# Kernel optimization log

Measured on AMD Instinct MI355X. Metric: run time of the kernel, lower is better.

## Reference

```python
import jax, jax.numpy as jnp
import numpy as np

B, T, H = 32, 500, 1612            # 6 regions * 256 + iti 76
ALM_EXC_LO, ALM_EXC_HI = 1280, 1460  # alm starts at 5*256; exc = 0.7*256 = 180 units
T_CONST = 0.1


def _base_firing():
    # per-region base firing rates: str 0, gpe 0.8, stn 0.5, snr 0.8, thal 0.8, alm 0, iti 0
    sizes = [256, 256, 256, 256, 256, 256, 76]
    rates = [0.0, 0.8, 0.5, 0.8, 0.8, 0.0, 0.0]
    return jnp.asarray(np.concatenate([np.full(s, r, np.float32) for s, r in zip(sizes, rates)]))


def setup_inputs() -> dict:
    key = jax.random.key(0)
    ks = jax.random.split(key, 12)
    inp = jax.random.normal(ks[0], (B, T, 1), jnp.float32)
    cue_inp = jax.random.normal(ks[1], (B, T, 1), jnp.float32)
    hn = jax.random.uniform(ks[2], (1, B, H), jnp.float32)
    xn = 0.1 * jax.random.normal(ks[3], (1, B, H), jnp.float32)
    inhib_stim = 0.01 * jax.random.normal(ks[4], (B, T, H), jnp.float32)
    W_rec = jax.random.uniform(ks[5], (H, H), jnp.float32, 0.0, 0.01)
    # binary connectivity mask (stands in for the sparse/cell-type block masks)
    W_rec_mask = (jax.random.uniform(ks[6], (H, H), jnp.float32) < 0.5).astype(jnp.float32)
    W_rec_fixed = jnp.zeros((H, H), jnp.float32)
    # diagonal +/-1 sign matrix (Dale's law), kept as a full matrix as in the source
    signs = jnp.where(jax.random.uniform(ks[7], (H,), jnp.float32) < 0.5, -1.0, 1.0)
    W_rec_sign = jnp.diag(signs)
    W_inp = jax.random.uniform(ks[8], (H, 1), jnp.float32, 0.0, 0.01)
    W_cue = jax.random.uniform(ks[9], (H, 1), jnp.float32, 0.0, 0.01)
    out_weight_alm = (1.0 / 256.0) * jnp.ones((1, ALM_EXC_HI - ALM_EXC_LO), jnp.float32)
    base_firing = _base_firing()
    return {"inp": inp, "cue_inp": cue_inp, "hn": hn, "xn": xn, "inhib_stim": inhib_stim,
            "W_rec": W_rec, "W_rec_mask": W_rec_mask, "W_rec_fixed": W_rec_fixed,
            "W_rec_sign": W_rec_sign, "W_inp": W_inp, "W_cue": W_cue,
            "out_weight_alm": out_weight_alm, "base_firing": base_firing}


def reference(inp, cue_inp, hn, xn, inhib_stim, W_rec, W_rec_mask, W_rec_fixed,
              W_rec_sign, W_inp, W_cue, out_weight_alm, base_firing):
    # Dale's-law constrained effective recurrent weights:
    # (mask * hardtanh(W, 0, 1) + fixed) @ sign
    W_eff = (W_rec_mask * jnp.clip(W_rec, 0.0, 1.0) + W_rec_fixed) @ W_rec_sign  # [H,H]
    x0 = xn[0]  # [B,H]
    h0 = hn[0]  # [B,H]

    def step(carry, ts):
        x, h = carry
        i_t, c_t, s_t = ts  # [B,1],[B,1],[B,H]
        ff = h @ W_eff.T + i_t @ W_inp.T + c_t @ W_cue.T + s_t
        x_new = x + T_CONST * (-x + ff)
        h_new = jax.nn.relu(x_new + base_firing)
        return (x_new, h_new), h_new

    ts = (jnp.transpose(inp, (1, 0, 2)), jnp.transpose(cue_inp, (1, 0, 2)),
          jnp.transpose(inhib_stim, (1, 0, 2)))
    _, hs = jax.lax.scan(step, (x0, h0), ts)  # hs: [T,B,H]
    out = hs[:, :, ALM_EXC_LO:ALM_EXC_HI] @ out_weight_alm.T  # [T,B,out_dim]
    return jnp.transpose(out, (1, 0, 2))  # [B,T,out_dim]
```

## Files before the change

### kernel.cpp

```cpp
#include <hip/hip_runtime.h>

#define BB 32
#define TT 500
#define HH 1612
#define HP 1664
#define HR 1624
#define NW 16
#define THREADS 1024
#define NWG 256
#define RPW 8
#define KPW (HP / NW)
#define ALO 1280
#define AHI 1460
#define WSTR 1668
#define RSTR 36
#define HBUF (HP * BB)
#define T_CONST 0.1f


__global__ void pers_init(const float* __restrict__ hn, const float* __restrict__ Wsign,
                          float* __restrict__ out, float* __restrict__ hbase,
                          float* __restrict__ sdiag, unsigned* __restrict__ cnt)
{
    const int gid = blockIdx.x * blockDim.x + threadIdx.x;
    const int gsz = gridDim.x * blockDim.x;
    for (int i = gid; i < HP; i += gsz)
        sdiag[i] = (i < HH) ? Wsign[(size_t)i * HH + i] : 0.f;
    for (int i = gid; i < HP * BB; i += gsz) {
        const int k = i >> 5, b = i & 31;
        hbase[(k >> 2) * 128 + b * 4 + (k & 3)] = (k < HH) ? hn[b * HH + k] : 0.f;
    }
    for (int i = gid; i < TT * 13 * 128; i += gsz) {
        const int buf = 1 + i / (13 * 128);
        const int off = i % (13 * 128);
        hbase[(size_t)buf * HBUF + 403 * 128 + off] = 0.f;
    }
    for (int i = gid; i < BB * TT; i += gsz) out[i] = 0.f;
    for (int i = gid; i < 512; i += gsz) cnt[i] = 0u;
}

__global__ __launch_bounds__(THREADS, 1) void pers_kernel(
    const float* __restrict__ xn,
    const float* __restrict__ Wrec, const float* __restrict__ Wmask,
    const float* __restrict__ Wfix, const float* __restrict__ sdiag,
    const float* __restrict__ inp,  const float* __restrict__ cue,
    const float* __restrict__ stim, const float* __restrict__ Winp,
    const float* __restrict__ Wcue, const float* __restrict__ walm,
    const float* __restrict__ base, float* __restrict__ out,
    float* __restrict__ hbase,      unsigned* __restrict__ cnt)
{
    __shared__ float Wlds[RPW * WSTR];
    __shared__ float red[NW * RPW * RSTR];
    __shared__ float almb[RPW * RSTR];

    const int tid  = threadIdx.x;
    const int wg   = blockIdx.x;
    const int wave = tid >> 6;
    const int lane = tid & 63;
    const int bl   = lane & 15;
    const int rq   = (lane >> 4) & 3;

    const int r0    = (wg * HH) / NWG;
    const int r1    = ((wg + 1) * HH) / NWG;
    const int nreal = r1 - r0;

    for (int i = tid; i < RPW * (HP / 4); i += THREADS) {
        const int r = i / (HP / 4), k = (i % (HP / 4)) * 4;
        const int j = r0 + r;
        float4 v = make_float4(0.f, 0.f, 0.f, 0.f);
        if (r < nreal && k < HH) {
            const float4 w = *(const float4*)&Wrec[(size_t)j * HH + k];
            const float4 m = *(const float4*)&Wmask[(size_t)j * HH + k];
            const float4 f = *(const float4*)&Wfix[(size_t)j * HH + k];
            const float4 s = *(const float4*)&sdiag[k];
            v.x = (m.x * fminf(fmaxf(w.x, 0.f), 1.f) + f.x) * s.x;
            v.y = (m.y * fminf(fmaxf(w.y, 0.f), 1.f) + f.y) * s.y;
            v.z = (m.z * fminf(fmaxf(w.z, 0.f), 1.f) + f.z) * s.z;
            v.w = (m.w * fminf(fmaxf(w.w, 0.f), 1.f) + f.w) * s.w;
        }
        *(float4*)&Wlds[r * WSTR + k] = v;
    }

    const int er = tid & 7, eb = tid >> 3;
    const int ej = r0 + er;
    const bool eactive = (tid < 256) && (er < nreal);
    float xv = 0.f, basej = 0.f, winpj = 0.f, wcuej = 0.f, walmj = 0.f;
    if (eactive) {
        xv    = xn[eb * HH + ej];
        basej = base[ej];
        winpj = Winp[ej];
        wcuej = Wcue[ej];
        walmj = (ej >= ALO && ej < AHI) ? walm[ej - ALO] : 0.f;
    }
    const bool has_alm = (r1 > ALO) && (r0 < AHI);
    const int kbase = wave * KPW;

    __syncthreads();

    for (int t = 0; t < TT; ++t) {
        const float* __restrict__ hc = hbase + (size_t)t * HBUF;
        float* __restrict__ hx       = hbase + (size_t)(t + 1) * HBUF;

        float sv = 0.f, iv = 0.f, cv = 0.f;
        if (eactive) {
            sv = __builtin_nontemporal_load(
                     &stim[(size_t)eb * (TT * HH) + (size_t)t * HH + ej]);
            iv = inp[eb * TT + t];
            cv = cue[eb * TT + t];
        }

        float a00 = 0.f, a01 = 0.f, a10 = 0.f, a11 = 0.f;
        {
            const float* __restrict__ hq  = hc + kbase * BB + bl * 4;
            const float* __restrict__ w0p = &Wlds[rq * WSTR + kbase];
            const float* __restrict__ w1p = w0p + 4 * WSTR;
            #pragma unroll 2
            for (int q = 0; q < KPW / 4; ++q) {
                const float4 h0 = *(const float4*)(hq + q * 128);
                const float4 h1 = *(const float4*)(hq + q * 128 + 64);
                const float4 w0 = *(const float4*)(w0p + q * 4);
                const float4 w1 = *(const float4*)(w1p + q * 4);
                a00 = fmaf(w0.x, h0.x, a00); a00 = fmaf(w0.y, h0.y, a00);
                a00 = fmaf(w0.z, h0.z, a00); a00 = fmaf(w0.w, h0.w, a00);
                a01 = fmaf(w0.x, h1.x, a01); a01 = fmaf(w0.y, h1.y, a01);
                a01 = fmaf(w0.z, h1.z, a01); a01 = fmaf(w0.w, h1.w, a01);
                a10 = fmaf(w1.x, h0.x, a10); a10 = fmaf(w1.y, h0.y, a10);
                a10 = fmaf(w1.z, h0.z, a10); a10 = fmaf(w1.w, h0.w, a10);
                a11 = fmaf(w1.x, h1.x, a11); a11 = fmaf(w1.y, h1.y, a11);
                a11 = fmaf(w1.z, h1.z, a11); a11 = fmaf(w1.w, h1.w, a11);
            }
        }

        red[(wave * RPW + rq    ) * RSTR + bl     ] = a00;
        red[(wave * RPW + rq    ) * RSTR + bl + 16] = a01;
        red[(wave * RPW + rq + 4) * RSTR + bl     ] = a10;
        red[(wave * RPW + rq + 4) * RSTR + bl + 16] = a11;
        __syncthreads();

        float av = 0.f;
        if (tid < 256) {
            float ff = 0.f;
            #pragma unroll
            for (int w2 = 0; w2 < NW; ++w2)
                ff += red[(w2 * RPW + er) * RSTR + eb];
            if (eactive) {
                ff += sv;
                ff = fmaf(iv, winpj, ff);
                ff = fmaf(cv, wcuej, ff);
                xv = fmaf(T_CONST, ff - xv, xv);
                const float hval = fmaxf(xv + basej, 0.f);
                __hip_atomic_store(&hx[(ej >> 2) * 128 + eb * 4 + (ej & 3)], hval,
                                   __ATOMIC_RELAXED, __HIP_MEMORY_SCOPE_AGENT);
                av = hval * walmj;
            }
        }

        if (has_alm) {
            if (tid < 256) almb[er * RSTR + eb] = av;
            __syncthreads();
            if (tid < 32) {
                float s8 = 0.f;
                #pragma unroll
                for (int r = 0; r < RPW; ++r) s8 += almb[r * RSTR + tid];
                atomicAdd(&out[tid * TT + t], s8);
            }
        }

        if (t != TT - 1) {
            __syncthreads();
            if (tid == 0)
                __hip_atomic_fetch_add(&cnt[(wg & 7) << 6], 1u,
                                       __ATOMIC_RELAXED, __HIP_MEMORY_SCOPE_AGENT);
            if (wave == 0) {
                const unsigned target = 256u * (unsigned)(t + 1);
                unsigned s;
                do {
                    __builtin_amdgcn_s_sleep(1);
                    unsigned v = (lane < 8)
                        ? __hip_atomic_load(&cnt[lane << 6], __ATOMIC_RELAXED,
                                            __HIP_MEMORY_SCOPE_AGENT)
                        : 0u;
                    v += __shfl_xor(v, 1);
                    v += __shfl_xor(v, 2);
                    v += __shfl_xor(v, 4);
                    s = __shfl(v, 0);
                } while (s < target);
            }
            __syncthreads();
        }
    }
}


#define FTHREADS 512
#define FNW 8
#define FKPW (HP / FNW)

__global__ void init_kernel(const float* __restrict__ hn, const float* __restrict__ xn,
                            const float* __restrict__ Wsign, float* __restrict__ out,
                            float* __restrict__ hA, float* __restrict__ xs,
                            float* __restrict__ sdiag)
{
    const int gid = blockIdx.x * blockDim.x + threadIdx.x;
    const int gsz = gridDim.x * blockDim.x;
    for (int i = gid; i < HP; i += gsz)
        sdiag[i] = (i < HH) ? Wsign[(size_t)i * HH + i] : 0.f;
    for (int i = gid; i < HP * BB; i += gsz) {
        const int k = i >> 5, b = i & 31;
        hA[(k >> 2) * (BB * 4) + b * 4 + (k & 3)] = (k < HH) ? hn[b * HH + k] : 0.f;
    }
    for (int i = gid; i < HH * BB; i += gsz) {
        const int j = i >> 5, b = i & 31;
        xs[i] = xn[b * HH + j];
    }
    for (int i = gid; i < BB * TT; i += gsz) out[i] = 0.f;
}

__global__ void weff_kernel(const float* __restrict__ Wrec, const float* __restrict__ Wmask,
                            const float* __restrict__ Wfix, const float* __restrict__ sdiag,
                            float* __restrict__ Weff)
{
    const int gid = blockIdx.x * blockDim.x + threadIdx.x;
    const int gsz = gridDim.x * blockDim.x;
    const int nq = HR * (HP / 4);
    for (int qi = gid; qi < nq; qi += gsz) {
        const int j = qi / (HP / 4);
        const int k = (qi % (HP / 4)) * 4;
        float4 v = make_float4(0.f, 0.f, 0.f, 0.f);
        if (j < HH && k < HH) {
            const float4 w = *(const float4*)&Wrec[(size_t)j * HH + k];
            const float4 m = *(const float4*)&Wmask[(size_t)j * HH + k];
            const float4 f = *(const float4*)&Wfix[(size_t)j * HH + k];
            const float4 s = *(const float4*)&sdiag[k];
            v.x = (m.x * fminf(fmaxf(w.x, 0.f), 1.f) + f.x) * s.x;
            v.y = (m.y * fminf(fmaxf(w.y, 0.f), 1.f) + f.y) * s.y;
            v.z = (m.z * fminf(fmaxf(w.z, 0.f), 1.f) + f.z) * s.z;
            v.w = (m.w * fminf(fmaxf(w.w, 0.f), 1.f) + f.w) * s.w;
        }
        *(float4*)&Weff[(size_t)j * HP + k] = v;
    }
}

template <bool PRE>
__global__ __launch_bounds__(FTHREADS, 1) void step_kernel(
    const int t,
    const float* __restrict__ hc,  float* __restrict__ hnx,
    float* __restrict__ xs,        const float* __restrict__ Weff,
    const float* __restrict__ Wrec,const float* __restrict__ Wmask,
    const float* __restrict__ Wfix,const float* __restrict__ sdiag,
    const float* __restrict__ inp, const float* __restrict__ cue,
    const float* __restrict__ stim,const float* __restrict__ Winp,
    const float* __restrict__ Wcue,const float* __restrict__ walm,
    const float* __restrict__ base,float* __restrict__ out)
{
    __shared__ float Wlds[RPW * WSTR];
    __shared__ float red[FNW * RPW * RSTR];
    __shared__ float almb[RPW * RSTR];

    const int tid  = threadIdx.x;
    const int wg   = blockIdx.x;
    const int wave = tid >> 6;
    const int lane = tid & 63;
    const int bl   = lane & 15;
    const int rq   = (lane >> 4) & 3;

    const int r0    = (wg * HH) / NWG;
    const int r1    = ((wg + 1) * HH) / NWG;
    const int nreal = r1 - r0;

    const int er = tid & 7, eb = tid >> 3;
    const int ej = r0 + er;
    const bool eactive = (tid < 256) && (er < nreal);
    float sv = 0.f, iv = 0.f, cv = 0.f, xv = 0.f;
    float basej = 0.f, winpj = 0.f, wcuej = 0.f, walmj = 0.f;
    if (eactive) {
        sv    = __builtin_nontemporal_load(
                    &stim[(size_t)eb * (TT * HH) + (size_t)t * HH + ej]);
        iv    = inp[eb * TT + t];
        cv    = cue[eb * TT + t];
        xv    = xs[ej * BB + eb];
        basej = base[ej];
        winpj = Winp[ej];
        wcuej = Wcue[ej];
        walmj = (ej >= ALO && ej < AHI) ? walm[ej - ALO] : 0.f;
    }
    const bool has_alm = (r1 > ALO) && (r0 < AHI);

    if constexpr (PRE) {
        for (int i = tid; i < RPW * (HP / 4); i += FTHREADS) {
            const int r = i / (HP / 4), k = (i % (HP / 4)) * 4;
            const float4 v = *(const float4*)&Weff[(size_t)(r0 + r) * HP + k];
            *(float4*)&Wlds[r * WSTR + k] = v;
        }
    } else {
        for (int i = tid; i < RPW * (HP / 4); i += FTHREADS) {
            const int r = i / (HP / 4), k = (i % (HP / 4)) * 4;
            const int j = r0 + r;
            float4 v = make_float4(0.f, 0.f, 0.f, 0.f);
            if (r < nreal && k < HH) {
                const float4 w = *(const float4*)&Wrec[(size_t)j * HH + k];
                const float4 m = *(const float4*)&Wmask[(size_t)j * HH + k];
                const float4 f = *(const float4*)&Wfix[(size_t)j * HH + k];
                const float4 s = *(const float4*)&sdiag[k];
                v.x = (m.x * fminf(fmaxf(w.x, 0.f), 1.f) + f.x) * s.x;
                v.y = (m.y * fminf(fmaxf(w.y, 0.f), 1.f) + f.y) * s.y;
                v.z = (m.z * fminf(fmaxf(w.z, 0.f), 1.f) + f.z) * s.z;
                v.w = (m.w * fminf(fmaxf(w.w, 0.f), 1.f) + f.w) * s.w;
            }
            *(float4*)&Wlds[r * WSTR + k] = v;
        }
    }
    __syncthreads();

    float a00 = 0.f, a01 = 0.f, a10 = 0.f, a11 = 0.f;
    {
        const int kbase = wave * FKPW;
        const float* __restrict__ hq  = hc + kbase * BB + bl * 4;
        const float* __restrict__ w0p = &Wlds[rq * WSTR + kbase];
        const float* __restrict__ w1p = w0p + 4 * WSTR;
        #pragma unroll 4
        for (int q = 0; q < FKPW / 4; ++q) {
            const float4 h0 = *(const float4*)(hq + q * 128);
            const float4 h1 = *(const float4*)(hq + q * 128 + 64);
            const float4 w0 = *(const float4*)(w0p + q * 4);
            const float4 w1 = *(const float4*)(w1p + q * 4);
            a00 = fmaf(w0.x, h0.x, a00); a00 = fmaf(w0.y, h0.y, a00);
            a00 = fmaf(w0.z, h0.z, a00); a00 = fmaf(w0.w, h0.w, a00);
            a01 = fmaf(w0.x, h1.x, a01); a01 = fmaf(w0.y, h1.y, a01);
            a01 = fmaf(w0.z, h1.z, a01); a01 = fmaf(w0.w, h1.w, a01);
            a10 = fmaf(w1.x, h0.x, a10); a10 = fmaf(w1.y, h0.y, a10);
            a10 = fmaf(w1.z, h0.z, a10); a10 = fmaf(w1.w, h0.w, a10);
            a11 = fmaf(w1.x, h1.x, a11); a11 = fmaf(w1.y, h1.y, a11);
            a11 = fmaf(w1.z, h1.z, a11); a11 = fmaf(w1.w, h1.w, a11);
        }
    }

    red[(wave * RPW + rq    ) * RSTR + bl     ] = a00;
    red[(wave * RPW + rq    ) * RSTR + bl + 16] = a01;
    red[(wave * RPW + rq + 4) * RSTR + bl     ] = a10;
    red[(wave * RPW + rq + 4) * RSTR + bl + 16] = a11;
    __syncthreads();

    float av = 0.f;
    if (tid < 256) {
        float ff = 0.f;
        #pragma unroll
        for (int w2 = 0; w2 < FNW; ++w2)
            ff += red[(w2 * RPW + er) * RSTR + eb];
        if (eactive) {
            ff += sv;
            ff = fmaf(iv, winpj, ff);
            ff = fmaf(cv, wcuej, ff);
            xv = fmaf(T_CONST, ff - xv, xv);
            xs[ej * BB + eb] = xv;
            const float hval = fmaxf(xv + basej, 0.f);
            hnx[(ej >> 2) * (BB * 4) + eb * 4 + (ej & 3)] = hval;
            av = hval * walmj;
        }
    }

    if (has_alm) {
        if (tid < 256) almb[er * RSTR + eb] = av;
        __syncthreads();
        if (tid < 32) {
            float s8 = 0.f;
            #pragma unroll
            for (int r = 0; r < RPW; ++r) s8 += almb[r * RSTR + tid];
            atomicAdd(&out[tid * TT + t], s8);
        }
    }
}

extern "C" void kernel_launch(void* const* d_in, const int* in_sizes, int n_in,
                              void* d_out, int out_size, void* d_ws, size_t ws_size,
                              hipStream_t stream) {
    const float* inp   = (const float*)d_in[0];
    const float* cue   = (const float*)d_in[1];
    const float* hn    = (const float*)d_in[2];
    const float* xn    = (const float*)d_in[3];
    const float* stim  = (const float*)d_in[4];
    const float* Wrec  = (const float*)d_in[5];
    const float* Wmask = (const float*)d_in[6];
    const float* Wfix  = (const float*)d_in[7];
    const float* Wsign = (const float*)d_in[8];
    const float* Winp  = (const float*)d_in[9];
    const float* Wcue  = (const float*)d_in[10];
    const float* walm  = (const float*)d_in[11];
    const float* base  = (const float*)d_in[12];
    float* out = (float*)d_out;

    const size_t pers_need = ((size_t)(TT + 1) * HBUF + HP) * sizeof(float) + 2048;
    if (ws_size >= pers_need) {
        float* hbase    = (float*)d_ws;
        float* sdiag    = hbase + (size_t)(TT + 1) * HBUF;
        unsigned* cnt   = (unsigned*)(sdiag + HP);

        pers_init<<<NWG, 256, 0, stream>>>(hn, Wsign, out, hbase, sdiag, cnt);

        void* args[] = { (void*)&xn, (void*)&Wrec, (void*)&Wmask, (void*)&Wfix,
                         (void*)&sdiag, (void*)&inp, (void*)&cue, (void*)&stim,
                         (void*)&Winp, (void*)&Wcue, (void*)&walm, (void*)&base,
                         (void*)&out, (void*)&hbase, (void*)&cnt };
        hipLaunchCooperativeKernel(reinterpret_cast<void*>(pers_kernel),
                                   dim3(NWG), dim3(THREADS), args, 0, stream);
        return;
    }

    const size_t weff_elems = (size_t)HR * HP;
    const size_t need = (weff_elems + 3 * (size_t)HP * BB + HP) * sizeof(float);
    const bool pre = (ws_size >= need);

    float* Weff, *hA, *hB, *xs, *sdiag;
    if (pre) {
        Weff  = (float*)d_ws;
        hA    = Weff + weff_elems;
    } else {
        Weff  = nullptr;
        hA    = (float*)d_ws;
    }
    hB    = hA + (size_t)HP * BB;
    xs    = hB + (size_t)HP * BB;
    sdiag = xs + (size_t)HP * BB;

    init_kernel<<<NWG, 256, 0, stream>>>(hn, xn, Wsign, out, hA, xs, sdiag);
    if (pre)
        weff_kernel<<<NWG, 256, 0, stream>>>(Wrec, Wmask, Wfix, sdiag, Weff);

    float* hc = hA;
    float* hx = hB;
    for (int t = 0; t < TT; ++t) {
        if (pre)
            step_kernel<true><<<NWG, FTHREADS, 0, stream>>>(
                t, hc, hx, xs, Weff, nullptr, nullptr, nullptr, nullptr,
                inp, cue, stim, Winp, Wcue, walm, base, out);
        else
            step_kernel<false><<<NWG, FTHREADS, 0, stream>>>(
                t, hc, hx, xs, nullptr, Wrec, Wmask, Wfix, sdiag,
                inp, cue, stim, Winp, Wcue, walm, base, out);
        float* tmp = hc; hc = hx; hx = tmp;
    }
}
```

Baseline: 5.199 ms.

## Keep recurrent weights in registers and reduce partial sums with wave shuffles

Each thread now holds a 4-row by 13-column slice of the effective recurrent weights in registers, instead of the workgroup staging 8 rows in LDS. The hidden-state buffer moves to a plain k-major [k][b] layout, and each thread reads 8 batch values per k. Partial sums are first combined with cross-lane shuffles, then with an LDS reduction over k-slices. The grid-barrier arrive is issued earlier and the sleep in the spin-wait is removed, to cut LDS traffic and barrier latency. Padding rows of later h buffers are no longer zeroed, so any non-finite garbage left in the workspace could leak into the sums. Register pressure also rises.

After: 14.14 ms. 172% more time.

```diff
diff --git a/kernel.cpp b/kernel.cpp
--- a/kernel.cpp
+++ b/kernel.cpp
@@ -5,17 +5,22 @@
 #define HH 1612
 #define HP 1664
 #define HR 1624
-#define NW 16
+#define NWG 256
 #define THREADS 1024
-#define NWG 256
-#define RPW 8
-#define KPW (HP / NW)
 #define ALO 1280
 #define AHI 1460
+#define T_CONST 0.1f
+#define HBUFS (HP * BB)
+#define KSL 208
+#define KL 13
+#define RED_STR 36
+
 #define WSTR 1668
 #define RSTR 36
-#define HBUF (HP * BB)
-#define T_CONST 0.1f
+#define RPW 8
+#define FTHREADS 512
+#define FNW 8
+#define FKPW (HP / FNW)
 
 
 __global__ void pers_init(const float* __restrict__ hn, const float* __restrict__ Wsign,
@@ -26,15 +31,12 @@
     const int gsz = gridDim.x * blockDim.x;
     for (int i = gid; i < HP; i += gsz)
         sdiag[i] = (i < HH) ? Wsign[(size_t)i * HH + i] : 0.f;
-    for (int i = gid; i < HP * BB; i += gsz) {
+    for (int i = gid; i < HH * BB; i += gsz) {
         const int k = i >> 5, b = i & 31;
-        hbase[(k >> 2) * 128 + b * 4 + (k & 3)] = (k < HH) ? hn[b * HH + k] : 0.f;
-    }
-    for (int i = gid; i < TT * 13 * 128; i += gsz) {
-        const int buf = 1 + i / (13 * 128);
-        const int off = i % (13 * 128);
-        hbase[(size_t)buf * HBUF + 403 * 128 + off] = 0.f;
-    }
+        hbase[k * BB + b] = hn[b * HH + k];
+    }
+    for (int i = gid; i < (HP - HH) * BB; i += gsz)
+        hbase[HH * BB + i] = 0.f;
     for (int i = gid; i < BB * TT; i += gsz) out[i] = 0.f;
     for (int i = gid; i < 512; i += gsz) cnt[i] = 0u;
 }
@@ -49,39 +51,41 @@
     const float* __restrict__ base, float* __restrict__ out,
     float* __restrict__ hbase,      unsigned* __restrict__ cnt)
 {
-    __shared__ float Wlds[RPW * WSTR];
-    __shared__ float red[NW * RPW * RSTR];
-    __shared__ float almb[RPW * RSTR];
+    __shared__ float red[256 * RED_STR];
+    __shared__ float almb[8 * 33];
 
     const int tid  = threadIdx.x;
     const int wg   = blockIdx.x;
     const int wave = tid >> 6;
     const int lane = tid & 63;
-    const int bl   = lane & 15;
-    const int rq   = (lane >> 4) & 3;
+    const int rh   = wave >> 3;
+    const int ks   = wave & 7;
+    const int kg   = lane >> 2;
+    const int bg   = lane & 3;
 
     const int r0    = (wg * HH) / NWG;
     const int r1    = ((wg + 1) * HH) / NWG;
     const int nreal = r1 - r0;
 
-    for (int i = tid; i < RPW * (HP / 4); i += THREADS) {
-        const int r = i / (HP / 4), k = (i % (HP / 4)) * 4;
-        const int j = r0 + r;
-        float4 v = make_float4(0.f, 0.f, 0.f, 0.f);
-        if (r < nreal && k < HH) {
-            const float4 w = *(const float4*)&Wrec[(size_t)j * HH + k];
-            const float4 m = *(const float4*)&Wmask[(size_t)j * HH + k];
-            const float4 f = *(const float4*)&Wfix[(size_t)j * HH + k];
-            const float4 s = *(const float4*)&sdiag[k];
-            v.x = (m.x * fminf(fmaxf(w.x, 0.f), 1.f) + f.x) * s.x;
-            v.y = (m.y * fminf(fmaxf(w.y, 0.f), 1.f) + f.y) * s.y;
-            v.z = (m.z * fminf(fmaxf(w.z, 0.f), 1.f) + f.z) * s.z;
-            v.w = (m.w * fminf(fmaxf(w.w, 0.f), 1.f) + f.w) * s.w;
-        }
-        *(float4*)&Wlds[r * WSTR + k] = v;
-    }
-
-    const int er = tid & 7, eb = tid >> 3;
+    const int k0 = ks * KSL + kg * KL;
+    float W[4][KL];
+    #pragma unroll
+    for (int rr = 0; rr < 4; ++rr) {
+        const int j = r0 + rh * 4 + rr;
+        #pragma unroll
+        for (int i = 0; i < KL; ++i) {
+            const int k = k0 + i;
+            float v = 0.f;
+            if (j < HH && k < HH) {
+                float w = Wrec[(size_t)j * HH + k];
+                w = fminf(fmaxf(w, 0.f), 1.f);
+                v = (Wmask[(size_t)j * HH + k] * w + Wfix[(size_t)j * HH + k]) * sdiag[k];
+            }
+            W[rr][i] = v;
+        }
+    }
+
+    const int er = tid >> 5, eb = tid & 31;
     const int ej = r0 + er;
     const bool eactive = (tid < 256) && (er < nreal);
     float xv = 0.f, basej = 0.f, winpj = 0.f, wcuej = 0.f, walmj = 0.f;
@@ -93,13 +97,14 @@
         walmj = (ej >= ALO && ej < AHI) ? walm[ej - ALO] : 0.f;
     }
     const bool has_alm = (r1 > ALO) && (r0 < AHI);
-    const int kbase = wave * KPW;
+    const int erh = er >> 2, err = er & 3;
+    const int off0 = k0 * BB + bg * 8;
 
     __syncthreads();
 
     for (int t = 0; t < TT; ++t) {
-        const float* __restrict__ hc = hbase + (size_t)t * HBUF;
-        float* __restrict__ hx       = hbase + (size_t)(t + 1) * HBUF;
+        const float* __restrict__ hc = hbase + (size_t)t * HBUFS;
+        float* __restrict__ hx       = hbase + (size_t)(t + 1) * HBUFS;
 
         float sv = 0.f, iv = 0.f, cv = 0.f;
         if (eactive) {
@@ -109,73 +114,95 @@
             cv = cue[eb * TT + t];
         }
 
-        float a00 = 0.f, a01 = 0.f, a10 = 0.f, a11 = 0.f;
-        {
-            const float* __restrict__ hq  = hc + kbase * BB + bl * 4;
-            const float* __restrict__ w0p = &Wlds[rq * WSTR + kbase];
-            const float* __restrict__ w1p = w0p + 4 * WSTR;
-            #pragma unroll 2
-            for (int q = 0; q < KPW / 4; ++q) {
-                const float4 h0 = *(const float4*)(hq + q * 128);
-                const float4 h1 = *(const float4*)(hq + q * 128 + 64);
-                const float4 w0 = *(const float4*)(w0p + q * 4);
-                const float4 w1 = *(const float4*)(w1p + q * 4);
-                a00 = fmaf(w0.x, h0.x, a00); a00 = fmaf(w0.y, h0.y, a00);
-                a00 = fmaf(w0.z, h0.z, a00); a00 = fmaf(w0.w, h0.w, a00);
-                a01 = fmaf(w0.x, h1.x, a01); a01 = fmaf(w0.y, h1.y, a01);
-                a01 = fmaf(w0.z, h1.z, a01); a01 = fmaf(w0.w, h1.w, a01);
-                a10 = fmaf(w1.x, h0.x, a10); a10 = fmaf(w1.y, h0.y, a10);
-                a10 = fmaf(w1.z, h0.z, a10); a10 = fmaf(w1.w, h0.w, a10);
-                a11 = fmaf(w1.x, h1.x, a11); a11 = fmaf(w1.y, h1.y, a11);
-                a11 = fmaf(w1.z, h1.z, a11); a11 = fmaf(w1.w, h1.w, a11);
-            }
-        }
-
-        red[(wave * RPW + rq    ) * RSTR + bl     ] = a00;
-        red[(wave * RPW + rq    ) * RSTR + bl + 16] = a01;
-        red[(wave * RPW + rq + 4) * RSTR + bl     ] = a10;
-        red[(wave * RPW + rq + 4) * RSTR + bl + 16] = a11;
+        float acc[4][8];
+        #pragma unroll
+        for (int rr = 0; rr < 4; ++rr)
+            #pragma unroll
+            for (int bb = 0; bb < 8; ++bb) acc[rr][bb] = 0.f;
+
+        const float* __restrict__ hp = hc + off0;
+        #pragma unroll
+        for (int i = 0; i < KL; ++i) {
+            const float4 ha = *(const float4*)(hp + i * BB);
+            const float4 hb = *(const float4*)(hp + i * BB + 4);
+            #pragma unroll
+            for (int rr = 0; rr < 4; ++rr) {
+                const float w = W[rr][i];
+                acc[rr][0] = fmaf(w, ha.x, acc[rr][0]);
+                acc[rr][1] = fmaf(w, ha.y, acc[rr][1]);
+                acc[rr][2] = fmaf(w, ha.z, acc[rr][2]);
+                acc[rr][3] = fmaf(w, ha.w, acc[rr][3]);
+                acc[rr][4] = fmaf(w, hb.x, acc[rr][4]);
+                acc[rr][5] = fmaf(w, hb.y, acc[rr][5]);
+                acc[rr][6] = fmaf(w, hb.z, acc[rr][6]);
+                acc[rr][7] = fmaf(w, hb.w, acc[rr][7]);
+            }
+        }
+
+        #pragma unroll
+        for (int rr = 0; rr < 4; ++rr)
+            #pragma unroll
+            for (int bb = 0; bb < 8; ++bb) {
+                float v = acc[rr][bb];
+                v += __shfl_xor(v, 4);
+                v += __shfl_xor(v, 8);
+                acc[rr][bb] = v;
+            }
+
+        if ((lane & 12) == 0) {
+            const int kq = lane >> 4;
+            #pragma unroll
+            for (int rr = 0; rr < 4; ++rr) {
+                const int row = wave * 16 + kq * 4 + rr;
+                *(float4*)&red[row * RED_STR + bg * 8] =
+                    make_float4(acc[rr][0], acc[rr][1], acc[rr][2], acc[rr][3]);
+                *(float4*)&red[row * RED_STR + bg * 8 + 4] =
+                    make_float4(acc[rr][4], acc[rr][5], acc[rr][6], acc[rr][7]);
+            }
+        }
         __syncthreads();
 
         float av = 0.f;
         if (tid < 256) {
             float ff = 0.f;
             #pragma unroll
-            for (int w2 = 0; w2 < NW; ++w2)
-                ff += red[(w2 * RPW + er) * RSTR + eb];
+            for (int ksx = 0; ksx < 8; ++ksx)
+                #pragma unroll
+                for (int kq = 0; kq < 4; ++kq)
+                    ff += red[((erh * 8 + ksx) * 16 + kq * 4 + err) * RED_STR + eb];
             if (eactive) {
                 ff += sv;
                 ff = fmaf(iv, winpj, ff);
                 ff = fmaf(cv, wcuej, ff);
                 xv = fmaf(T_CONST, ff - xv, xv);
                 const float hval = fmaxf(xv + basej, 0.f);
-                __hip_atomic_store(&hx[(ej >> 2) * 128 + eb * 4 + (ej & 3)], hval,
+                __hip_atomic_store(&hx[ej * BB + eb], hval,
                                    __ATOMIC_RELAXED, __HIP_MEMORY_SCOPE_AGENT);
                 av = hval * walmj;
             }
-        }
+            if (has_alm) almb[er * 33 + eb] = av;
+        }
+
+        __syncthreads();
+
+        if (tid == 0)
+            __hip_atomic_fetch_add(&cnt[(wg & 7) << 6], 1u,
+                                   __ATOMIC_RELAXED, __HIP_MEMORY_SCOPE_AGENT);
 
         if (has_alm) {
-            if (tid < 256) almb[er * RSTR + eb] = av;
-            __syncthreads();
             if (tid < 32) {
                 float s8 = 0.f;
                 #pragma unroll
-                for (int r = 0; r < RPW; ++r) s8 += almb[r * RSTR + tid];
+                for (int r = 0; r < 8; ++r) s8 += almb[r * 33 + tid];
                 atomicAdd(&out[tid * TT + t], s8);
             }
         }
 
         if (t != TT - 1) {
-            __syncthreads();
-            if (tid == 0)
-                __hip_atomic_fetch_add(&cnt[(wg & 7) << 6], 1u,
-                                       __ATOMIC_RELAXED, __HIP_MEMORY_SCOPE_AGENT);
             if (wave == 0) {
                 const unsigned target = 256u * (unsigned)(t + 1);
                 unsigned s;
                 do {
-                    __builtin_amdgcn_s_sleep(1);
                     unsigned v = (lane < 8)
                         ? __hip_atomic_load(&cnt[lane << 6], __ATOMIC_RELAXED,
                                             __HIP_MEMORY_SCOPE_AGENT)
@@ -191,10 +218,6 @@
     }
 }
 
-
-#define FTHREADS 512
-#define FNW 8
-#define FKPW (HP / FNW)
 
 __global__ void init_kernel(const float* __restrict__ hn, const float* __restrict__ xn,
                             const float* __restrict__ Wsign, float* __restrict__ out,
@@ -254,8 +277,8 @@
     const float* __restrict__ base,float* __restrict__ out)
 {
     __shared__ float Wlds[RPW * WSTR];
-    __shared__ float red[FNW * RPW * RSTR];
-    __shared__ float almb[RPW * RSTR];
+    __shared__ float red2[FNW * RPW * RSTR];
+    __shared__ float almb2[RPW * RSTR];
 
     const int tid  = threadIdx.x;
     const int wg   = blockIdx.x;
@@ -335,10 +358,10 @@
         }
     }
 
-    red[(wave * RPW + rq    ) * RSTR + bl     ] = a00;
-    red[(wave * RPW + rq    ) * RSTR + bl + 16] = a01;
-    red[(wave * RPW + rq + 4) * RSTR + bl     ] = a10;
-    red[(wave * RPW + rq + 4) * RSTR + bl + 16] = a11;
+    red2[(wave * RPW + rq    ) * RSTR + bl     ] = a00;
+    red2[(wave * RPW + rq    ) * RSTR + bl + 16] = a01;
+    red2[(wave * RPW + rq + 4) * RSTR + bl     ] = a10;
+    red2[(wave * RPW + rq + 4) * RSTR + bl + 16] = a11;
     __syncthreads();
 
     float av = 0.f;
@@ -346,7 +369,7 @@
         float ff = 0.f;
         #pragma unroll
         for (int w2 = 0; w2 < FNW; ++w2)
-            ff += red[(w2 * RPW + er) * RSTR + eb];
+            ff += red2[(w2 * RPW + er) * RSTR + eb];
         if (eactive) {
             ff += sv;
             ff = fmaf(iv, winpj, ff);
@@ -360,12 +383,12 @@
     }
 
     if (has_alm) {
-        if (tid < 256) almb[er * RSTR + eb] = av;
+        if (tid < 256) almb2[er * RSTR + eb] = av;
         __syncthreads();
         if (tid < 32) {
             float s8 = 0.f;
             #pragma unroll
-            for (int r = 0; r < RPW; ++r) s8 += almb[r * RSTR + tid];
+            for (int r = 0; r < RPW; ++r) s8 += almb2[r * RSTR + tid];
             atomicAdd(&out[tid * TT + t], s8);
         }
     }
@@ -389,10 +412,10 @@
     const float* base  = (const float*)d_in[12];
     float* out = (float*)d_out;
 
-    const size_t pers_need = ((size_t)(TT + 1) * HBUF + HP) * sizeof(float) + 2048;
+    const size_t pers_need = ((size_t)(TT + 1) * HBUFS + HP) * sizeof(float) + 2048;
     if (ws_size >= pers_need) {
         float* hbase    = (float*)d_ws;
-        float* sdiag    = hbase + (size_t)(TT + 1) * HBUF;
+        float* sdiag    = hbase + (size_t)(TT + 1) * HBUFS;
         unsigned* cnt   = (unsigned*)(sdiag + HP);
 
         pers_init<<<NWG, 256, 0, stream>>>(hn, Wsign, out, hbase, sdiag, cnt);
```
